# Kernel optimization log

Measured on AMD Instinct MI355X. Metric: run time of the kernel, lower is better.

Reference implementation:

```python
import jax, jax.numpy as jnp
import numpy as np

N_NODES = 100000

def setup_inputs() -> dict:
    key = jax.random.key(0)
    k1, k2, k3, k4, k5 = jax.random.split(key, 5)
    E = 1600000
    feat = jax.random.normal(k1, (N_NODES, 128), dtype=jnp.float32)
    W = jax.random.normal(k2, (128, 32), dtype=jnp.float32) * 0.08  # ~xavier scale
    edge_w = jax.random.uniform(k3, (E,), dtype=jnp.float32)
    src = jax.random.randint(k4, (E,), 0, N_NODES, dtype=jnp.int32)
    dst = jax.random.randint(k5, (E,), 0, N_NODES, dtype=jnp.int32)
    return {"feat": feat, "W": W, "edge_w": edge_w, "src": src, "dst": dst}

def reference(feat, W, edge_w, src, dst):
    # linear transform: [N, in] @ [in, out] -> [N, out]
    h = feat @ W
    # gather source features per edge, scale by edge weight: u_mul_e
    m = h[src] * edge_w[:, None]  # [E, out]
    # sum messages at destination nodes
    rst = jax.ops.segment_sum(m, dst, num_segments=N_NODES)  # [N, out]
    return rst
```

## Files before the change

### kernel.cpp

```cpp
#include <hip/hip_runtime.h>
#include <hip/hip_fp16.h>

constexpr int N_IN    = 128;
constexpr int N_OUT   = 32;
constexpr int LOG_R   = 6;
constexpr int RANGE   = 1 << LOG_R;
constexpr int MAXNB   = 2048;
constexpr int NCC     = 256;
constexpr int PBLK    = 512;
constexpr int CHUNK_P = 2048;

union H4 { uint2 u; __half2 h2[2]; };

__global__ __launch_bounds__(256) void gemm_h(
    const float* __restrict__ feat, const float* __restrict__ W,
    __half* __restrict__ h, int n)
{
    __shared__ float Ws[N_IN * N_OUT];
    for (int i = threadIdx.x; i < (N_IN * N_OUT) / 4; i += 256)
        reinterpret_cast<float4*>(Ws)[i] = reinterpret_cast<const float4*>(W)[i];
    __syncthreads();

    int gid = blockIdx.x * 256 + threadIdx.x;
    int row = gid >> 3;
    if (row >= n) return;
    int cg = (gid & 7) * 4;

    const float4* frow = reinterpret_cast<const float4*>(feat + (size_t)row * N_IN);
    float4 acc = make_float4(0.f, 0.f, 0.f, 0.f);
    #pragma unroll
    for (int k4 = 0; k4 < N_IN / 4; ++k4) {
        float4 f = frow[k4];
        int k = k4 * 4;
        float4 w0 = *reinterpret_cast<const float4*>(&Ws[(k + 0) * N_OUT + cg]);
        float4 w1 = *reinterpret_cast<const float4*>(&Ws[(k + 1) * N_OUT + cg]);
        float4 w2 = *reinterpret_cast<const float4*>(&Ws[(k + 2) * N_OUT + cg]);
        float4 w3 = *reinterpret_cast<const float4*>(&Ws[(k + 3) * N_OUT + cg]);
        acc.x += f.x * w0.x + f.y * w1.x + f.z * w2.x + f.w * w3.x;
        acc.y += f.x * w0.y + f.y * w1.y + f.z * w2.y + f.w * w3.y;
        acc.z += f.x * w0.z + f.y * w1.z + f.z * w2.z + f.w * w3.z;
        acc.w += f.x * w0.w + f.y * w1.w + f.z * w2.w + f.w * w3.w;
    }
    H4 v;
    v.h2[0] = __float22half2_rn(make_float2(acc.x, acc.y));
    v.h2[1] = __float22half2_rn(make_float2(acc.z, acc.w));
    *reinterpret_cast<uint2*>(h + (size_t)row * N_OUT + cg) = v.u;
}

__global__ __launch_bounds__(PBLK) void partition2_k(
    const int* __restrict__ src, const int* __restrict__ dst,
    const float* __restrict__ w, int* __restrict__ tbl,
    int2* __restrict__ sw, int E, int NB, int epc)
{
    __shared__ int hist[MAXNB];
    __shared__ int wscan[PBLK];

    const int c   = blockIdx.x;
    const int tid = threadIdx.x;
    const int e0  = c * epc;
    const int e1  = min(e0 + epc, E);
    const int m   = max(e1 - e0, 0);
    const int slots = (NB + PBLK - 1) / PBLK;

    for (int i = tid; i < NB; i += PBLK) hist[i] = 0;
    __syncthreads();

    for (int e = e0 + tid; e < e1; e += PBLK)
        atomicAdd(&hist[dst[e] >> LOG_R], 1);
    __syncthreads();

    int tsum = 0;
    int base = tid * slots;
    for (int j = 0; j < slots; ++j) {
        int idx = base + j;
        if (idx < NB) tsum += hist[idx];
    }
    wscan[tid] = tsum;
    __syncthreads();
    for (int off = 1; off < PBLK; off <<= 1) {
        int x = (tid >= off) ? wscan[tid - off] : 0;
        __syncthreads();
        wscan[tid] += x;
        __syncthreads();
    }
    int run = wscan[tid] - tsum;
    __syncthreads();
    for (int j = 0; j < slots; ++j) {
        int idx = base + j;
        if (idx < NB) {
            int cval = hist[idx];
            tbl[(size_t)c * (NB + 1) + idx] = run;
            hist[idx] = run;
            run += cval;
        }
    }
    if (tid == 0) tbl[(size_t)c * (NB + 1) + NB] = m;
    __syncthreads();

    int2* outp = sw + (size_t)c * epc;
    for (int e = e0 + tid; e < e1; e += PBLK) {
        int d   = dst[e];
        int b   = d >> LOG_R;
        int loc = d & (RANGE - 1);
        int pos = atomicAdd(&hist[b], 1);
        outp[pos] = make_int2(src[e] | (loc << 17), __float_as_int(w[e]));
    }
}

__global__ __launch_bounds__(256) void conv3_k(
    const __half* __restrict__ h, const int2* __restrict__ sw,
    const int* __restrict__ tbl, float* __restrict__ out,
    int n, int NB, int ncc, int epc)
{
    __shared__ int2 pairs[CHUNK_P];
    __shared__ unsigned short order[CHUNK_P];
    __shared__ int cnt[RANGE];
    __shared__ int sc[RANGE];
    __shared__ int start[RANGE + 1];
    __shared__ int cur[RANGE];
    __shared__ int rs[NCC];
    __shared__ int ps[NCC + 1];
    __shared__ int stmp[256];

    const int b   = blockIdx.x;
    const int tid = threadIdx.x;
    const int g   = tid >> 3;
    const int cg  = (tid & 7) * 4;

    int len = 0;
    if (tid < ncc) {
        int s0 = tbl[(size_t)tid * (NB + 1) + b];
        int s1 = tbl[(size_t)tid * (NB + 1) + b + 1];
        rs[tid] = s0;
        len = s1 - s0;
    }
    stmp[tid] = len;
    __syncthreads();
    for (int off = 1; off < 256; off <<= 1) {
        int x = (tid >= off) ? stmp[tid - off] : 0;
        __syncthreads();
        stmp[tid] += x;
        __syncthreads();
    }
    ps[tid + 1] = stmp[tid];
    if (tid == 0) ps[0] = 0;
    __syncthreads();
    const int deg = ps[ncc];

    float4 accA = make_float4(0.f, 0.f, 0.f, 0.f);
    float4 accB = make_float4(0.f, 0.f, 0.f, 0.f);

    for (int cbase = 0; cbase < deg; cbase += CHUNK_P) {
        const int m = min(CHUNK_P, deg - cbase);

        for (int i = tid; i < m; i += 256) {
            int gidx = cbase + i;
            int lo = 0, hi = ncc - 1;
            while (lo < hi) {
                int mid = (lo + hi + 1) >> 1;
                if (ps[mid] <= gidx) lo = mid; else hi = mid - 1;
            }
            int off = gidx - ps[lo];
            pairs[i] = sw[(size_t)lo * epc + rs[lo] + off];
        }
        if (tid < RANGE) cnt[tid] = 0;
        __syncthreads();

        for (int i = tid; i < m; i += 256)
            atomicAdd(&cnt[pairs[i].x >> 17], 1);
        __syncthreads();

        int v = 0;
        if (tid < RANGE) { v = cnt[tid]; sc[tid] = v; }
        __syncthreads();
        #pragma unroll
        for (int off = 1; off < RANGE; off <<= 1) {
            int x = (tid < RANGE && tid >= off) ? sc[tid - off] : 0;
            __syncthreads();
            if (tid < RANGE) sc[tid] += x;
            __syncthreads();
        }
        if (tid < RANGE) { start[tid] = sc[tid] - v; cur[tid] = sc[tid] - v; }
        if (tid == RANGE - 1) start[RANGE] = sc[RANGE - 1];
        __syncthreads();

        for (int i = tid; i < m; i += 256) {
            int loc = pairs[i].x >> 17;
            int pos = atomicAdd(&cur[loc], 1);
            order[pos] = (unsigned short)i;
        }
        __syncthreads();

        int k  = start[2 * g];
        int ke = start[2 * g + 2];
        #define LOAD_H(p, f01, f23)                                            \
            H4 _u##f01;                                                        \
            _u##f01.u = *reinterpret_cast<const uint2*>(                       \
                h + (size_t)((p).x & 0x1FFFF) * N_OUT + cg);                   \
            float2 f01 = __half22float2(_u##f01.h2[0]);                        \
            float2 f23 = __half22float2(_u##f01.h2[1]);
        #define ACC_STEP(p, f01, f23)                                          \
        {                                                                      \
            float wv  = __int_as_float((p).y);                                 \
            int   odd = ((p).x >> 17) & 1;                                     \
            float wa = odd ? 0.f : wv, wb = odd ? wv : 0.f;                    \
            accA.x += f01.x * wa; accA.y += f01.y * wa;                        \
            accA.z += f23.x * wa; accA.w += f23.y * wa;                        \
            accB.x += f01.x * wb; accB.y += f01.y * wb;                        \
            accB.z += f23.x * wb; accB.w += f23.y * wb;                        \
        }
        for (; k + 3 < ke; k += 4) {
            int i0 = order[k + 0], i1 = order[k + 1];
            int i2 = order[k + 2], i3 = order[k + 3];
            int2 p0 = pairs[i0], p1 = pairs[i1], p2 = pairs[i2], p3 = pairs[i3];
            LOAD_H(p0, a01, a23)
            LOAD_H(p1, b01, b23)
            LOAD_H(p2, c01, c23)
            LOAD_H(p3, d01, d23)
            ACC_STEP(p0, a01, a23)
            ACC_STEP(p1, b01, b23)
            ACC_STEP(p2, c01, c23)
            ACC_STEP(p3, d01, d23)
        }
        for (; k < ke; ++k) {
            int i = order[k];
            int2 p = pairs[i];
            LOAD_H(p, e01, e23)
            ACC_STEP(p, e01, e23)
        }
        #undef LOAD_H
        #undef ACC_STEP
        __syncthreads();
    }

    const int lo2 = b * RANGE;
    int node0 = lo2 + 2 * g;
    if (node0 < n)
        *reinterpret_cast<float4*>(out + (size_t)node0 * N_OUT + cg) = accA;
    if (node0 + 1 < n)
        *reinterpret_cast<float4*>(out + (size_t)(node0 + 1) * N_OUT + cg) = accB;
}

__global__ __launch_bounds__(256) void fused_edge(
    const float* __restrict__ feat, const float* __restrict__ W,
    const float* __restrict__ edge_w, const int* __restrict__ src,
    const int* __restrict__ dst, float* __restrict__ out, int E)
{
    __shared__ float Ws[N_IN * N_OUT];
    for (int i = threadIdx.x; i < (N_IN * N_OUT) / 4; i += 256)
        reinterpret_cast<float4*>(Ws)[i] = reinterpret_cast<const float4*>(W)[i];
    __syncthreads();
    int gid = blockIdx.x * 256 + threadIdx.x;
    int e = gid >> 3;
    if (e >= E) return;
    int cg = (gid & 7) * 4;
    int s = src[e];
    int d = dst[e];
    float w = edge_w[e];
    const float4* frow = reinterpret_cast<const float4*>(feat + (size_t)s * N_IN);
    float4 acc = make_float4(0.f, 0.f, 0.f, 0.f);
    #pragma unroll
    for (int k4 = 0; k4 < N_IN / 4; ++k4) {
        float4 f = frow[k4];
        int k = k4 * 4;
        float4 w0 = *reinterpret_cast<const float4*>(&Ws[(k + 0) * N_OUT + cg]);
        float4 w1 = *reinterpret_cast<const float4*>(&Ws[(k + 1) * N_OUT + cg]);
        float4 w2 = *reinterpret_cast<const float4*>(&Ws[(k + 2) * N_OUT + cg]);
        float4 w3 = *reinterpret_cast<const float4*>(&Ws[(k + 3) * N_OUT + cg]);
        acc.x += f.x * w0.x + f.y * w1.x + f.z * w2.x + f.w * w3.x;
        acc.y += f.x * w0.y + f.y * w1.y + f.z * w2.y + f.w * w3.y;
        acc.z += f.x * w0.z + f.y * w1.z + f.z * w2.z + f.w * w3.z;
        acc.w += f.x * w0.w + f.y * w1.w + f.z * w2.w + f.w * w3.w;
    }
    float* o = out + (size_t)d * N_OUT + cg;
    atomicAdd(o + 0, acc.x * w);
    atomicAdd(o + 1, acc.y * w);
    atomicAdd(o + 2, acc.z * w);
    atomicAdd(o + 3, acc.w * w);
}

extern "C" void kernel_launch(void* const* d_in, const int* in_sizes, int n_in,
                              void* d_out, int out_size, void* d_ws, size_t ws_size,
                              hipStream_t stream) {
    const float* feat   = (const float*)d_in[0];
    const float* W      = (const float*)d_in[1];
    const float* edge_w = (const float*)d_in[2];
    const int*   src    = (const int*)d_in[3];
    const int*   dst    = (const int*)d_in[4];
    float* out = (float*)d_out;

    int n = in_sizes[0] / N_IN;
    int E = in_sizes[2];

    int NB  = (n + RANGE - 1) / RANGE;
    int ncc = NCC;
    int epc = (E + ncc - 1) / ncc;

    size_t off_h   = 0;
    size_t off_tbl = (off_h + (size_t)n * N_OUT * sizeof(__half) + 15) & ~(size_t)15;
    size_t off_sw  = (off_tbl + (size_t)ncc * (NB + 1) * sizeof(int) + 15) & ~(size_t)15;
    size_t need    = off_sw + (size_t)ncc * epc * sizeof(int2);

    bool ok = (ws_size >= need) && (n <= (1 << 17)) && (NB <= MAXNB);

    if (ok) {
        char* ws = (char*)d_ws;
        __half* h  = (__half*)(ws + off_h);
        int*   tbl = (int*)(ws + off_tbl);
        int2*  sw  = (int2*)(ws + off_sw);

        long gthreads = (long)n * 8;
        gemm_h<<<(int)((gthreads + 255) / 256), 256, 0, stream>>>(feat, W, h, n);
        partition2_k<<<ncc, PBLK, 0, stream>>>(src, dst, edge_w, tbl, sw, E, NB, epc);
        conv3_k<<<NB, 256, 0, stream>>>(h, sw, tbl, out, n, NB, ncc, epc);
    } else {
        hipError_t _e = hipMemsetAsync(d_out, 0, (size_t)out_size * sizeof(float), stream);
        (void)_e;
        long sthreads = (long)E * 8;
        fused_edge<<<(int)((sthreads + 255) / 256), 256, 0, stream>>>(feat, W, edge_w, src, dst, out, E);
    }
}
```

Measured before the change: 80.33 us.

## Vectorize partition loads and add single-chunk fast path with physical sort in conv

```diff
diff --git a/kernel.cpp b/kernel.cpp
--- a/kernel.cpp
+++ b/kernel.cpp
@@ -60,13 +60,20 @@
     const int e0  = c * epc;
     const int e1  = min(e0 + epc, E);
     const int m   = max(e1 - e0, 0);
+    const int m4  = m & ~3;
     const int slots = (NB + PBLK - 1) / PBLK;
 
     for (int i = tid; i < NB; i += PBLK) hist[i] = 0;
     __syncthreads();
 
-    for (int e = e0 + tid; e < e1; e += PBLK)
-        atomicAdd(&hist[dst[e] >> LOG_R], 1);
+    for (int o = tid * 4; o < m4; o += PBLK * 4) {
+        int4 dv = *reinterpret_cast<const int4*>(dst + e0 + o);
+        atomicAdd(&hist[dv.x >> LOG_R], 1);
+        atomicAdd(&hist[dv.y >> LOG_R], 1);
+        atomicAdd(&hist[dv.z >> LOG_R], 1);
+        atomicAdd(&hist[dv.w >> LOG_R], 1);
+    }
+    if (m4 + tid < m) atomicAdd(&hist[dst[e0 + m4 + tid] >> LOG_R], 1);
     __syncthreads();
 
     int tsum = 0;
@@ -98,22 +105,34 @@
     __syncthreads();
 
     int2* outp = sw + (size_t)c * epc;
-    for (int e = e0 + tid; e < e1; e += PBLK) {
-        int d   = dst[e];
-        int b   = d >> LOG_R;
-        int loc = d & (RANGE - 1);
-        int pos = atomicAdd(&hist[b], 1);
-        outp[pos] = make_int2(src[e] | (loc << 17), __float_as_int(w[e]));
-    }
-}
-
-__global__ __launch_bounds__(256) void conv3_k(
+    for (int o = tid * 4; o < m4; o += PBLK * 4) {
+        int4   sv = *reinterpret_cast<const int4*>(src + e0 + o);
+        int4   dv = *reinterpret_cast<const int4*>(dst + e0 + o);
+        float4 wv = *reinterpret_cast<const float4*>(w + e0 + o);
+        int p0 = atomicAdd(&hist[dv.x >> LOG_R], 1);
+        int p1 = atomicAdd(&hist[dv.y >> LOG_R], 1);
+        int p2 = atomicAdd(&hist[dv.z >> LOG_R], 1);
+        int p3 = atomicAdd(&hist[dv.w >> LOG_R], 1);
+        outp[p0] = make_int2(sv.x | ((dv.x & (RANGE - 1)) << 17), __float_as_int(wv.x));
+        outp[p1] = make_int2(sv.y | ((dv.y & (RANGE - 1)) << 17), __float_as_int(wv.y));
+        outp[p2] = make_int2(sv.z | ((dv.z & (RANGE - 1)) << 17), __float_as_int(wv.z));
+        outp[p3] = make_int2(sv.w | ((dv.w & (RANGE - 1)) << 17), __float_as_int(wv.w));
+    }
+    if (m4 + tid < m) {
+        int e = e0 + m4 + tid;
+        int d = dst[e];
+        int pos = atomicAdd(&hist[d >> LOG_R], 1);
+        outp[pos] = make_int2(src[e] | ((d & (RANGE - 1)) << 17), __float_as_int(w[e]));
+    }
+}
+
+__global__ __launch_bounds__(256) void conv4_k(
     const __half* __restrict__ h, const int2* __restrict__ sw,
     const int* __restrict__ tbl, float* __restrict__ out,
     int n, int NB, int ncc, int epc)
 {
     __shared__ int2 pairs[CHUNK_P];
-    __shared__ unsigned short order[CHUNK_P];
+    __shared__ int2 pairs_s[CHUNK_P];
     __shared__ int cnt[RANGE];
     __shared__ int sc[RANGE];
     __shared__ int start[RANGE + 1];
@@ -150,24 +169,37 @@
     float4 accA = make_float4(0.f, 0.f, 0.f, 0.f);
     float4 accB = make_float4(0.f, 0.f, 0.f, 0.f);
 
-    for (int cbase = 0; cbase < deg; cbase += CHUNK_P) {
-        const int m = min(CHUNK_P, deg - cbase);
-
-        for (int i = tid; i < m; i += 256) {
-            int gidx = cbase + i;
-            int lo = 0, hi = ncc - 1;
-            while (lo < hi) {
-                int mid = (lo + hi + 1) >> 1;
-                if (ps[mid] <= gidx) lo = mid; else hi = mid - 1;
-            }
-            int off = gidx - ps[lo];
-            pairs[i] = sw[(size_t)lo * epc + rs[lo] + off];
-        }
+    #define LOAD_H(p, f01, f23)                                                \
+        H4 _u##f01;                                                            \
+        _u##f01.u = *reinterpret_cast<const uint2*>(                           \
+            h + (size_t)((p).x & 0x1FFFF) * N_OUT + cg);                       \
+        float2 f01 = __half22float2(_u##f01.h2[0]);                            \
+        float2 f23 = __half22float2(_u##f01.h2[1]);
+    #define ACC_STEP(p, f01, f23)                                              \
+    {                                                                          \
+        float wv  = __int_as_float((p).y);                                     \
+        int   odd = ((p).x >> 17) & 1;                                         \
+        float wa = odd ? 0.f : wv, wb = odd ? wv : 0.f;                        \
+        accA.x += f01.x * wa; accA.y += f01.y * wa;                            \
+        accA.z += f23.x * wa; accA.w += f23.y * wa;                            \
+        accB.x += f01.x * wb; accB.y += f01.y * wb;                            \
+        accB.z += f23.x * wb; accB.w += f23.y * wb;                            \
+    }
+
+    if (deg <= CHUNK_P) {
         if (tid < RANGE) cnt[tid] = 0;
         __syncthreads();
 
-        for (int i = tid; i < m; i += 256)
-            atomicAdd(&cnt[pairs[i].x >> 17], 1);
+        if (tid < ncc) {
+            int d0 = ps[tid];
+            int l  = ps[tid + 1] - d0;
+            const int2* sp = sw + (size_t)tid * epc + rs[tid];
+            for (int j = 0; j < l; ++j) {
+                int2 p = sp[j];
+                pairs[d0 + j] = p;
+                atomicAdd(&cnt[p.x >> 17], 1);
+            }
+        }
         __syncthreads();
 
         int v = 0;
@@ -184,35 +216,18 @@
         if (tid == RANGE - 1) start[RANGE] = sc[RANGE - 1];
         __syncthreads();
 
-        for (int i = tid; i < m; i += 256) {
-            int loc = pairs[i].x >> 17;
-            int pos = atomicAdd(&cur[loc], 1);
-            order[pos] = (unsigned short)i;
+        for (int i = tid; i < deg; i += 256) {
+            int2 p = pairs[i];
+            int pos = atomicAdd(&cur[p.x >> 17], 1);
+            pairs_s[pos] = p;
         }
         __syncthreads();
 
         int k  = start[2 * g];
         int ke = start[2 * g + 2];
-        #define LOAD_H(p, f01, f23)                                            \
-            H4 _u##f01;                                                        \
-            _u##f01.u = *reinterpret_cast<const uint2*>(                       \
-                h + (size_t)((p).x & 0x1FFFF) * N_OUT + cg);                   \
-            float2 f01 = __half22float2(_u##f01.h2[0]);                        \
-            float2 f23 = __half22float2(_u##f01.h2[1]);
-        #define ACC_STEP(p, f01, f23)                                          \
-        {                                                                      \
-            float wv  = __int_as_float((p).y);                                 \
-            int   odd = ((p).x >> 17) & 1;                                     \
-            float wa = odd ? 0.f : wv, wb = odd ? wv : 0.f;                    \
-            accA.x += f01.x * wa; accA.y += f01.y * wa;                        \
-            accA.z += f23.x * wa; accA.w += f23.y * wa;                        \
-            accB.x += f01.x * wb; accB.y += f01.y * wb;                        \
-            accB.z += f23.x * wb; accB.w += f23.y * wb;                        \
-        }
         for (; k + 3 < ke; k += 4) {
-            int i0 = order[k + 0], i1 = order[k + 1];
-            int i2 = order[k + 2], i3 = order[k + 3];
-            int2 p0 = pairs[i0], p1 = pairs[i1], p2 = pairs[i2], p3 = pairs[i3];
+            int2 p0 = pairs_s[k + 0], p1 = pairs_s[k + 1];
+            int2 p2 = pairs_s[k + 2], p3 = pairs_s[k + 3];
             LOAD_H(p0, a01, a23)
             LOAD_H(p1, b01, b23)
             LOAD_H(p2, c01, c23)
@@ -223,15 +238,64 @@
             ACC_STEP(p3, d01, d23)
         }
         for (; k < ke; ++k) {
-            int i = order[k];
-            int2 p = pairs[i];
+            int2 p = pairs_s[k];
             LOAD_H(p, e01, e23)
             ACC_STEP(p, e01, e23)
         }
-        #undef LOAD_H
-        #undef ACC_STEP
-        __syncthreads();
-    }
+    } else {
+        for (int cbase = 0; cbase < deg; cbase += CHUNK_P) {
+            const int m = min(CHUNK_P, deg - cbase);
+
+            for (int i = tid; i < m; i += 256) {
+                int gidx = cbase + i;
+                int lo = 0, hi = ncc - 1;
+                while (lo < hi) {
+                    int mid = (lo + hi + 1) >> 1;
+                    if (ps[mid] <= gidx) lo = mid; else hi = mid - 1;
+                }
+                int off = gidx - ps[lo];
+                pairs[i] = sw[(size_t)lo * epc + rs[lo] + off];
+            }
+            if (tid < RANGE) cnt[tid] = 0;
+            __syncthreads();
+
+            for (int i = tid; i < m; i += 256)
+                atomicAdd(&cnt[pairs[i].x >> 17], 1);
+            __syncthreads();
+
+            int v = 0;
+            if (tid < RANGE) { v = cnt[tid]; sc[tid] = v; }
+            __syncthreads();
+            #pragma unroll
+            for (int off = 1; off < RANGE; off <<= 1) {
+                int x = (tid < RANGE && tid >= off) ? sc[tid - off] : 0;
+                __syncthreads();
+                if (tid < RANGE) sc[tid] += x;
+                __syncthreads();
+            }
+            if (tid < RANGE) { start[tid] = sc[tid] - v; cur[tid] = sc[tid] - v; }
+            if (tid == RANGE - 1) start[RANGE] = sc[RANGE - 1];
+            __syncthreads();
+
+            for (int i = tid; i < m; i += 256) {
+                int2 p = pairs[i];
+                int pos = atomicAdd(&cur[p.x >> 17], 1);
+                pairs_s[pos] = p;
+            }
+            __syncthreads();
+
+            int k  = start[2 * g];
+            int ke = start[2 * g + 2];
+            for (; k < ke; ++k) {
+                int2 p = pairs_s[k];
+                LOAD_H(p, f01, f23)
+                ACC_STEP(p, f01, f23)
+            }
+            __syncthreads();
+        }
+    }
+    #undef LOAD_H
+    #undef ACC_STEP
 
     const int lo2 = b * RANGE;
     int node0 = lo2 + 2 * g;
@@ -294,7 +358,7 @@
 
     int NB  = (n + RANGE - 1) / RANGE;
     int ncc = NCC;
-    int epc = (E + ncc - 1) / ncc;
+    int epc = (((E + ncc - 1) / ncc) + 3) & ~3;
 
     size_t off_h   = 0;
     size_t off_tbl = (off_h + (size_t)n * N_OUT * sizeof(__half) + 15) & ~(size_t)15;
@@ -312,7 +376,7 @@
         long gthreads = (long)n * 8;
         gemm_h<<<(int)((gthreads + 255) / 256), 256, 0, stream>>>(feat, W, h, n);
         partition2_k<<<ncc, PBLK, 0, stream>>>(src, dst, edge_w, tbl, sw, E, NB, epc);
-        conv3_k<<<NB, 256, 0, stream>>>(h, sw, tbl, out, n, NB, ncc, epc);
+        conv4_k<<<NB, 256, 0, stream>>>(h, sw, tbl, out, n, NB, ncc, epc);
     } else {
         hipError_t _e = hipMemsetAsync(d_out, 0, (size_t)out_size * sizeof(float), stream);
         (void)_e;
```

Measured after the change: 78.65 us. 2.1% less time.
